# Performance work log

Measured on AMD Instinct MI355X. Metric: run time of the kernel, lower is better.

## Reference

```python
import jax, jax.numpy as jnp
import numpy as np

# static config (matches init_kwargs)
DIM = 192; NUM_HEAD = 6; HEAD_DIM = DIM // NUM_HEAD
WIN = 8; WS = WIN * WIN            # win_seq = 64
B = 2; H = 256; Wd = 256
RH = H // WIN; RW = Wd // WIN; L = RH * RW   # 32x32 = 1024 windows
P = (2 * WIN - 1) ** 2             # 225 relative positions
SCALE = HEAD_DIM ** -0.5


def _relative_index():
    # same math as get_relative_index (torch.meshgrid default = 'ij')
    coords = np.stack(np.meshgrid(np.arange(WIN), np.arange(WIN), indexing='ij'))
    cf = coords.reshape(2, -1)
    rel = (cf[:, :, None] - cf[:, None, :]).transpose(1, 2, 0).copy()
    rel[:, :, 0] += WIN - 1
    rel[:, :, 1] += WIN - 1
    rel[:, :, 0] *= 2 * WIN - 1
    return rel.sum(-1).reshape(-1)  # (WS*WS,), values in [0, P)

POS_INDEX = jnp.asarray(_relative_index())


def _table_nb(rh, rw):
    # reflect-pad(1) + 3x3 unfold of window-id table -> neighbor window ids (L, 9)
    t = np.arange(rh * rw).reshape(rh, rw)
    tp = np.pad(t, 1, mode='reflect')
    nb = np.stack([tp[kh:kh + rh, kw:kw + rw] for kh in range(3) for kw in range(3)], axis=-1)
    return nb.reshape(rh * rw, 9)

TABLE_NB = jnp.asarray(_table_nb(RH, RW))  # (L, 9) int


def _unfold9(x):
    # x: (B, C, rh, rw) -> (B, L, C, 9); reflect pad 1 + 3x3 neighborhoods
    rh, rw = x.shape[2], x.shape[3]
    xp = jnp.pad(x, ((0, 0), (0, 0), (1, 1), (1, 1)), mode='reflect')
    nb = jnp.stack([xp[:, :, kh:kh + rh, kw:kw + rw] for kh in range(3) for kw in range(3)], axis=-1)
    return nb.reshape(x.shape[0], x.shape[1], rh * rw, 9).transpose(0, 2, 1, 3)


def _router(q, k, pos_embedding):
    # router runs on detached q, k (q.detach() in source)
    qd = jax.lax.stop_gradient(q)
    kd = jax.lax.stop_gradient(k)
    qr = qd.reshape(B, DIM, RH, WIN, RW, WIN).mean(axis=(3, 5))
    kr = kd.reshape(B, DIM, RH, WIN, RW, WIN).mean(axis=(3, 5))
    qr_flat = qr.reshape(B, DIM, L).transpose(0, 2, 1)      # (B, L, C)
    kr_fold = _unfold9(kr)                                   # (B, L, C, 9)
    a_r = jnp.einsum('blc,blcn->bln', qr_flat, kr_fold)      # routing scores
    a_r = a_r.at[..., 4].add(-100.0)                          # exclude self window
    # softmax is monotone -> argmax of a_r equals argmax of softmax(a_r)
    idx = jnp.argmax(a_r, axis=-1)                            # (B, L) in [0,9)
    idx_reflect = TABLE_NB[jnp.arange(L)[None, :], idx]       # (B, L) routed window id
    itself = pos_embedding[4]                                 # (nh, P)
    dirb = pos_embedding[idx]                                 # (B, L, nh, P)
    itself_b = itself[:, POS_INDEX].reshape(NUM_HEAD, WS, WS)
    itself_b = jnp.broadcast_to(itself_b, (B, L, NUM_HEAD, WS, WS))
    dir_b = dirb[..., POS_INDEX].reshape(B, L, NUM_HEAD, WS, WS)
    pos_embed = jnp.concatenate([itself_b, dir_b], axis=-1)   # (B, L, nh, WS, 2*WS)
    return idx_reflect, pos_embed


def reference(x, pos_embedding):
    # x: (B, 3*DIM, H, W) fused qkv feature map
    qc = x[:, :DIM]
    kc = x[:, DIM:2 * DIM]
    idx, pos_embed = _router(qc, kc, pos_embedding)
    # winP: window partition into (3, B, L, nh, WS, hd)
    qkv = x.reshape(B, 3, NUM_HEAD, HEAD_DIM, RH, WIN, RW, WIN)
    qkv = qkv.transpose(1, 0, 4, 6, 2, 5, 7, 3).reshape(3, B, L, NUM_HEAD, WS, HEAD_DIM)
    q, k, v = qkv[0], qkv[1], qkv[2]
    gather = jax.vmap(lambda a, i: a[i])     # per-batch window gather along L
    k_d = gather(k, idx)                     # (B, L, nh, WS, hd)
    v_d = gather(v, idx)
    k_g = jnp.concatenate([k, k_d], axis=3)  # (B, L, nh, 2*WS, hd)
    v_g = jnp.concatenate([v, v_d], axis=3)
    attn = jnp.einsum('blhsd,blhtd->blhst', q, k_g) * SCALE + pos_embed
    attn = jax.nn.softmax(attn, axis=-1)
    out = jnp.einsum('blhst,blhtd->blhsd', attn, v_g)  # (B, L, nh, WS, hd)
    # winR: window reverse to (B, DIM, H, W)
    out = out.reshape(B, RH, RW, NUM_HEAD, WIN, WIN, HEAD_DIM)
    out = out.transpose(0, 3, 6, 1, 4, 2, 5).reshape(B, DIM, H, Wd)
    return out


def setup_inputs() -> dict:
    key = jax.random.key(0)
    k1, k2 = jax.random.split(key)
    x = jax.random.normal(k1, (B, 3 * DIM, H, Wd), dtype=jnp.float32)
    pos_embedding = jax.random.normal(k2, (9, NUM_HEAD, P), dtype=jnp.float32) * 0.02
    return {"x": x, "pos_embedding": pos_embedding}
```

## Files before the change

kernel.cpp:

```cpp
#include <hip/hip_runtime.h>
#include <math.h>

namespace {
constexpr int cB   = 2;
constexpr int cDIM = 192;
constexpr int cNH  = 6;
constexpr int cHD  = 32;
constexpr int cWS  = 64;
constexpr int cH   = 256;
constexpr int cW   = 256;
constexpr int cRH  = 32;
constexpr int cL   = 1024;
constexpr int cP   = 225;
constexpr float cSCALE = 0.17677669529663688f;
}

__global__ void pool_kernel(const float* __restrict__ x, float* __restrict__ pool) {
    int blk = blockIdx.x;
    int rh = blk & 31;
    int c  = (blk >> 5) % 384;
    int b  = blk / (384 * 32);
    int tid = threadIdx.x;
    int i  = tid >> 5;
    int rw = tid & 31;
    const float* row = x + (((size_t)(b * 576 + c)) * cH + rh * 8 + i) * cW + rw * 8;
    float4 a0 = *(const float4*)row;
    float4 a1 = *(const float4*)(row + 4);
    float s = a0.x + a0.y + a0.z + a0.w + a1.x + a1.y + a1.z + a1.w;
    __shared__ float red[8][33];
    red[i][rw] = s;
    __syncthreads();
    if (tid < 32) {
        float t = 0.f;
        #pragma unroll
        for (int k = 0; k < 8; ++k) t += red[k][tid];
        pool[((size_t)(b * cL) + rh * 32 + tid) * 384 + c] = t * (1.0f / 64.0f);
    }
}

__global__ void router_kernel(const float* __restrict__ pool, int* __restrict__ idxbuf) {
    int blk = blockIdx.x;
    int l = blk & (cL - 1);
    int b = blk >> 10;
    int rh = l >> 5, rw = l & 31;
    int lane = threadIdx.x;
    int ln[9];
    #pragma unroll
    for (int n = 0; n < 9; ++n) {
        int nh = rh + n / 3 - 1;
        int nw = rw + n % 3 - 1;
        nh = nh < 0 ? 1 : (nh > 31 ? 30 : nh);
        nw = nw < 0 ? 1 : (nw > 31 ? 30 : nw);
        ln[n] = nh * 32 + nw;
    }
    float acc[9] = {0,0,0,0,0,0,0,0,0};
    const float* qb = pool + ((size_t)(b * cL) + l) * 384;
    #pragma unroll
    for (int ci = 0; ci < 3; ++ci) {
        int c = lane + ci * 64;
        float q = qb[c];
        #pragma unroll
        for (int n = 0; n < 9; ++n)
            acc[n] += q * pool[((size_t)(b * cL) + ln[n]) * 384 + 192 + c];
    }
    #pragma unroll
    for (int n = 0; n < 9; ++n)
        #pragma unroll
        for (int off = 32; off > 0; off >>= 1)
            acc[n] += __shfl_down(acc[n], off);
    if (lane == 0) {
        acc[4] -= 100.0f;
        int bi = 0; float bv = acc[0];
        #pragma unroll
        for (int n = 1; n < 9; ++n) if (acc[n] > bv) { bv = acc[n]; bi = n; }
        idxbuf[blk * 2]     = bi;
        idxbuf[blk * 2 + 1] = ln[bi];
    }
}

__global__ __launch_bounds__(256, 2) void attn_kernel(
    const float* __restrict__ x, const float* __restrict__ pe,
    const int* __restrict__ idxbuf, float* __restrict__ out)
{
    __shared__ float smem[12996];
    float* Vs  = smem;
    float* Qs  = smem + 4096;
    float* Ks  = smem + 6144;
    float* Ps  = smem + 4096;
    float* pes = smem + 12544;

    int blk = blockIdx.x;
    int h  = blk >> 11;
    int bl = blk & 2047;
    int b  = bl >> 10;
    int l  = bl & 1023;
    int rh = l >> 5, rw = l & 31;
    int tid = threadIdx.x;

    int dir  = idxbuf[bl * 2];
    int lwin = idxbuf[bl * 2 + 1];
    int rh2 = lwin >> 5, rw2 = lwin & 31;

    const float* pe_self = pe + (4 * cNH + h) * cP;
    const float* pe_dir  = pe + (dir * cNH + h) * cP;
    for (int t = tid; t < 2 * cP; t += 256)
        pes[t] = (t < cP) ? pe_self[t] : pe_dir[t - cP];

    {
        int d = tid & 31;
        int i = tid >> 5;
        int dsw = (d + 4 * i) & 31;
        const size_t CHW = (size_t)cH * cW;
        const float* xb = x + (size_t)b * (3 * cDIM) * CHW;
        size_t off_self = (size_t)(rh  * 8 + i) * cW + rw  * 8;
        size_t off_dir  = (size_t)(rh2 * 8 + i) * cW + rw2 * 8;
        size_t cq = (size_t)(h * cHD + d) * CHW;
        size_t ck = cq + (size_t)cDIM * CHW;
        size_t cv = ck + (size_t)cDIM * CHW;
        const float* srcs[5] = { xb + cq + off_self, xb + ck + off_self, xb + ck + off_dir,
                                 xb + cv + off_self, xb + cv + off_dir };
        float* dsts[5] = { Qs, Ks, Ks + 2048, Vs, Vs + 2048 };
        #pragma unroll
        for (int m = 0; m < 5; ++m) {
            float4 a0 = *(const float4*)(srcs[m]);
            float4 a1 = *(const float4*)(srcs[m] + 4);
            float vv[8] = {a0.x,a0.y,a0.z,a0.w,a1.x,a1.y,a1.z,a1.w};
            float mult = (m == 0) ? cSCALE : 1.0f;
            float* dd = dsts[m] + dsw;
            #pragma unroll
            for (int j = 0; j < 8; ++j)
                dd[(i * 8 + j) * 32] = vv[j] * mult;
        }
    }
    __syncthreads();

    int sg = tid >> 4;
    int tg = tid & 15;
    int s0 = sg * 4;
    int t0 = tg * 8;
    int si = s0 >> 3;
    int sj0 = s0 & 7;

    float sc[4][8];
    {
        const float* peb = pes + ((t0 < 64) ? 0 : cP);
        #pragma unroll
        for (int bb = 0; bb < 8; ++bb) {
            int tw = (t0 + bb) & 63;
            int ti = tw >> 3, tj = tw & 7;
            #pragma unroll
            for (int a = 0; a < 4; ++a)
                sc[a][bb] = peb[(si - ti + 7) * 15 + (sj0 + a - tj + 7)];
        }
    }

    int qc = 4 * (sg >> 1);
    int kc = (4 * tg) & 31;
    #pragma unroll
    for (int d4 = 0; d4 < 32; d4 += 4) {
        float4 qv[4], kv[8];
        #pragma unroll
        for (int a = 0; a < 4; ++a)
            qv[a] = *(const float4*)&Qs[(s0 + a) * 32 + ((d4 + qc) & 31)];
        #pragma unroll
        for (int bb = 0; bb < 8; ++bb)
            kv[bb] = *(const float4*)&Ks[(t0 + bb) * 32 + ((d4 + kc) & 31)];
        #pragma unroll
        for (int a = 0; a < 4; ++a)
            #pragma unroll
            for (int bb = 0; bb < 8; ++bb)
                sc[a][bb] += qv[a].x * kv[bb].x + qv[a].y * kv[bb].y
                           + qv[a].z * kv[bb].z + qv[a].w * kv[bb].w;
    }
    __syncthreads();

    #pragma unroll
    for (int a = 0; a < 4; ++a) {
        float m = sc[a][0];
        #pragma unroll
        for (int bb = 1; bb < 8; ++bb) m = fmaxf(m, sc[a][bb]);
        #pragma unroll
        for (int mask = 1; mask < 16; mask <<= 1) m = fmaxf(m, __shfl_xor(m, mask));
        float ssum = 0.f;
        #pragma unroll
        for (int bb = 0; bb < 8; ++bb) { sc[a][bb] = __expf(sc[a][bb] - m); ssum += sc[a][bb]; }
        #pragma unroll
        for (int mask = 1; mask < 16; mask <<= 1) ssum += __shfl_xor(ssum, mask);
        float r = 1.0f / ssum;
        #pragma unroll
        for (int bb = 0; bb < 8; ++bb) sc[a][bb] *= r;
        *(float4*)&Ps[(s0 + a) * 132 + t0]     = make_float4(sc[a][0], sc[a][1], sc[a][2], sc[a][3]);
        *(float4*)&Ps[(s0 + a) * 132 + t0 + 4] = make_float4(sc[a][4], sc[a][5], sc[a][6], sc[a][7]);
    }
    __syncthreads();

    int d0 = tg * 2;
    float oa0[4] = {0,0,0,0}, oa1[4] = {0,0,0,0};
    for (int t4 = 0; t4 < 128; t4 += 4) {
        int vc = (d0 + 4 * (t4 >> 3)) & 31;
        float4 pv[4];
        #pragma unroll
        for (int a = 0; a < 4; ++a)
            pv[a] = *(const float4*)&Ps[(s0 + a) * 132 + t4];
        float2 vv[4];
        #pragma unroll
        for (int u = 0; u < 4; ++u)
            vv[u] = *(const float2*)&Vs[(t4 + u) * 32 + vc];
        #pragma unroll
        for (int a = 0; a < 4; ++a) {
            oa0[a] += pv[a].x * vv[0].x + pv[a].y * vv[1].x + pv[a].z * vv[2].x + pv[a].w * vv[3].x;
            oa1[a] += pv[a].x * vv[0].y + pv[a].y * vv[1].y + pv[a].z * vv[2].y + pv[a].w * vv[3].y;
        }
    }

    const size_t CHW = (size_t)cH * cW;
    float* ob = out + (size_t)(b * cDIM + h * cHD) * CHW + (size_t)(rh * 8 + si) * cW + rw * 8 + sj0;
    *(float4*)(ob + (size_t)(d0    ) * CHW) = make_float4(oa0[0], oa0[1], oa0[2], oa0[3]);
    *(float4*)(ob + (size_t)(d0 + 1) * CHW) = make_float4(oa1[0], oa1[1], oa1[2], oa1[3]);
}

extern "C" void kernel_launch(void* const* d_in, const int* in_sizes, int n_in,
                              void* d_out, int out_size, void* d_ws, size_t ws_size,
                              hipStream_t stream) {
    const float* x  = (const float*)d_in[0];
    const float* pe = (const float*)d_in[1];
    float* out = (float*)d_out;
    float* pool   = (float*)d_ws;
    int*   idxbuf = (int*)((char*)d_ws + (size_t)cB * cL * 384 * sizeof(float));

    hipLaunchKernelGGL(pool_kernel,   dim3(cB * 384 * cRH), dim3(256), 0, stream, x, pool);
    hipLaunchKernelGGL(router_kernel, dim3(cB * cL),        dim3(64),  0, stream, pool, idxbuf);
    hipLaunchKernelGGL(attn_kernel,   dim3(cNH * cB * cL),  dim3(256), 0, stream, x, pe, idxbuf, out);
}
```

Measured before the change: 656.0 us.

## Use fp16 MFMA for window attention QK and PV products

Replaces the scalar fp32 QK^T and PV loops in the attention kernel with fp16 MFMA 16x16x32 instructions. Q, K and V are staged into shared memory as fp16 (V transposed), and the probability tile is kept per wave. The relative-position bias is loaded directly into the MFMA accumulator, which drops one block barrier. Shared memory shrinks and the launch bound rises to 3 blocks per CU. The cost is reduced precision in the fp16 operands and stores to the output that are no longer vectorized, since each lane now writes scalars.

```diff
diff --git a/kernel.cpp b/kernel.cpp
--- a/kernel.cpp
+++ b/kernel.cpp
@@ -6,7 +6,6 @@
 constexpr int cDIM = 192;
 constexpr int cNH  = 6;
 constexpr int cHD  = 32;
-constexpr int cWS  = 64;
 constexpr int cH   = 256;
 constexpr int cW   = 256;
 constexpr int cRH  = 32;
@@ -14,6 +13,10 @@
 constexpr int cP   = 225;
 constexpr float cSCALE = 0.17677669529663688f;
 }
+
+typedef _Float16 h8 __attribute__((ext_vector_type(8)));
+typedef _Float16 h4 __attribute__((ext_vector_type(4)));
+typedef float    f4 __attribute__((ext_vector_type(4)));
 
 __global__ void pool_kernel(const float* __restrict__ x, float* __restrict__ pool) {
     int blk = blockIdx.x;
@@ -78,16 +81,15 @@
     }
 }
 
-__global__ __launch_bounds__(256, 2) void attn_kernel(
+__global__ __launch_bounds__(256, 3) void attn_kernel(
     const float* __restrict__ x, const float* __restrict__ pe,
     const int* __restrict__ idxbuf, float* __restrict__ out)
 {
-    __shared__ float smem[12996];
-    float* Vs  = smem;
-    float* Qs  = smem + 4096;
-    float* Ks  = smem + 6144;
-    float* Ps  = smem + 4096;
-    float* pes = smem + 12544;
+    __shared__ _Float16 Qh[64 * 40];
+    __shared__ _Float16 Kh[128 * 40];
+    __shared__ _Float16 Vt[32 * 136];
+    __shared__ _Float16 Pst[4][16 * 136];
+    __shared__ float    pes[2 * cP];
 
     int blk = blockIdx.x;
     int h  = blk >> 11;
@@ -109,7 +111,6 @@
     {
         int d = tid & 31;
         int i = tid >> 5;
-        int dsw = (d + 4 * i) & 31;
         const size_t CHW = (size_t)cH * cW;
         const float* xb = x + (size_t)b * (3 * cDIM) * CHW;
         size_t off_self = (size_t)(rh  * 8 + i) * cW + rw  * 8;
@@ -117,106 +118,113 @@
         size_t cq = (size_t)(h * cHD + d) * CHW;
         size_t ck = cq + (size_t)cDIM * CHW;
         size_t cv = ck + (size_t)cDIM * CHW;
-        const float* srcs[5] = { xb + cq + off_self, xb + ck + off_self, xb + ck + off_dir,
-                                 xb + cv + off_self, xb + cv + off_dir };
-        float* dsts[5] = { Qs, Ks, Ks + 2048, Vs, Vs + 2048 };
-        #pragma unroll
-        for (int m = 0; m < 5; ++m) {
-            float4 a0 = *(const float4*)(srcs[m]);
-            float4 a1 = *(const float4*)(srcs[m] + 4);
+
+        {
+            float4 a0 = *(const float4*)(xb + cq + off_self);
+            float4 a1 = *(const float4*)(xb + cq + off_self + 4);
             float vv[8] = {a0.x,a0.y,a0.z,a0.w,a1.x,a1.y,a1.z,a1.w};
-            float mult = (m == 0) ? cSCALE : 1.0f;
-            float* dd = dsts[m] + dsw;
             #pragma unroll
             for (int j = 0; j < 8; ++j)
-                dd[(i * 8 + j) * 32] = vv[j] * mult;
+                Qh[(i * 8 + j) * 40 + d] = (_Float16)(vv[j] * cSCALE);
         }
+        {
+            float4 a0 = *(const float4*)(xb + ck + off_self);
+            float4 a1 = *(const float4*)(xb + ck + off_self + 4);
+            float vv[8] = {a0.x,a0.y,a0.z,a0.w,a1.x,a1.y,a1.z,a1.w};
+            #pragma unroll
+            for (int j = 0; j < 8; ++j)
+                Kh[(i * 8 + j) * 40 + d] = (_Float16)vv[j];
+            float4 b0 = *(const float4*)(xb + ck + off_dir);
+            float4 b1 = *(const float4*)(xb + ck + off_dir + 4);
+            float ww[8] = {b0.x,b0.y,b0.z,b0.w,b1.x,b1.y,b1.z,b1.w};
+            #pragma unroll
+            for (int j = 0; j < 8; ++j)
+                Kh[(64 + i * 8 + j) * 40 + d] = (_Float16)ww[j];
+        }
+        {
+            float4 a0 = *(const float4*)(xb + cv + off_self);
+            float4 a1 = *(const float4*)(xb + cv + off_self + 4);
+            h8 hv = { (_Float16)a0.x,(_Float16)a0.y,(_Float16)a0.z,(_Float16)a0.w,
+                      (_Float16)a1.x,(_Float16)a1.y,(_Float16)a1.z,(_Float16)a1.w };
+            *(h8*)&Vt[d * 136 + i * 8] = hv;
+            float4 b0 = *(const float4*)(xb + cv + off_dir);
+            float4 b1 = *(const float4*)(xb + cv + off_dir + 4);
+            h8 hw = { (_Float16)b0.x,(_Float16)b0.y,(_Float16)b0.z,(_Float16)b0.w,
+                      (_Float16)b1.x,(_Float16)b1.y,(_Float16)b1.z,(_Float16)b1.w };
+            *(h8*)&Vt[d * 136 + 64 + i * 8] = hw;
+        }
     }
     __syncthreads();
 
-    int sg = tid >> 4;
-    int tg = tid & 15;
-    int s0 = sg * 4;
-    int t0 = tg * 8;
-    int si = s0 >> 3;
-    int sj0 = s0 & 7;
-
-    float sc[4][8];
-    {
-        const float* peb = pes + ((t0 < 64) ? 0 : cP);
-        #pragma unroll
-        for (int bb = 0; bb < 8; ++bb) {
-            int tw = (t0 + bb) & 63;
-            int ti = tw >> 3, tj = tw & 7;
-            #pragma unroll
-            for (int a = 0; a < 4; ++a)
-                sc[a][bb] = peb[(si - ti + 7) * 15 + (sj0 + a - tj + 7)];
-        }
-    }
-
-    int qc = 4 * (sg >> 1);
-    int kc = (4 * tg) & 31;
-    #pragma unroll
-    for (int d4 = 0; d4 < 32; d4 += 4) {
-        float4 qv[4], kv[8];
-        #pragma unroll
-        for (int a = 0; a < 4; ++a)
-            qv[a] = *(const float4*)&Qs[(s0 + a) * 32 + ((d4 + qc) & 31)];
-        #pragma unroll
-        for (int bb = 0; bb < 8; ++bb)
-            kv[bb] = *(const float4*)&Ks[(t0 + bb) * 32 + ((d4 + kc) & 31)];
-        #pragma unroll
-        for (int a = 0; a < 4; ++a)
-            #pragma unroll
-            for (int bb = 0; bb < 8; ++bb)
-                sc[a][bb] += qv[a].x * kv[bb].x + qv[a].y * kv[bb].y
-                           + qv[a].z * kv[bb].z + qv[a].w * kv[bb].w;
-    }
-    __syncthreads();
-
-    #pragma unroll
-    for (int a = 0; a < 4; ++a) {
-        float m = sc[a][0];
-        #pragma unroll
-        for (int bb = 1; bb < 8; ++bb) m = fmaxf(m, sc[a][bb]);
-        #pragma unroll
-        for (int mask = 1; mask < 16; mask <<= 1) m = fmaxf(m, __shfl_xor(m, mask));
-        float ssum = 0.f;
-        #pragma unroll
-        for (int bb = 0; bb < 8; ++bb) { sc[a][bb] = __expf(sc[a][bb] - m); ssum += sc[a][bb]; }
-        #pragma unroll
-        for (int mask = 1; mask < 16; mask <<= 1) ssum += __shfl_xor(ssum, mask);
-        float r = 1.0f / ssum;
-        #pragma unroll
-        for (int bb = 0; bb < 8; ++bb) sc[a][bb] *= r;
-        *(float4*)&Ps[(s0 + a) * 132 + t0]     = make_float4(sc[a][0], sc[a][1], sc[a][2], sc[a][3]);
-        *(float4*)&Ps[(s0 + a) * 132 + t0 + 4] = make_float4(sc[a][4], sc[a][5], sc[a][6], sc[a][7]);
-    }
-    __syncthreads();
-
-    int d0 = tg * 2;
-    float oa0[4] = {0,0,0,0}, oa1[4] = {0,0,0,0};
-    for (int t4 = 0; t4 < 128; t4 += 4) {
-        int vc = (d0 + 4 * (t4 >> 3)) & 31;
-        float4 pv[4];
-        #pragma unroll
-        for (int a = 0; a < 4; ++a)
-            pv[a] = *(const float4*)&Ps[(s0 + a) * 132 + t4];
-        float2 vv[4];
-        #pragma unroll
-        for (int u = 0; u < 4; ++u)
-            vv[u] = *(const float2*)&Vs[(t4 + u) * 32 + vc];
-        #pragma unroll
-        for (int a = 0; a < 4; ++a) {
-            oa0[a] += pv[a].x * vv[0].x + pv[a].y * vv[1].x + pv[a].z * vv[2].x + pv[a].w * vv[3].x;
-            oa1[a] += pv[a].x * vv[0].y + pv[a].y * vv[1].y + pv[a].z * vv[2].y + pv[a].w * vv[3].y;
-        }
+    int lane = tid & 63;
+    int w    = tid >> 6;
+    int g    = lane >> 4;
+    int sl   = lane & 15;
+    int s_global = w * 16 + sl;
+
+    int base0 = ((s_global >> 3) + 7) * 15 + (s_global & 7) + 7;
+    int offs[4];
+    #pragma unroll
+    for (int q = 0; q < 4; ++q) {
+        int gq = 4 * g + q;
+        offs[q] = (gq >> 3) * 15 + (gq & 7);
+    }
+
+    h8 qf = *(const h8*)&Qh[s_global * 40 + g * 8];
+    f4 ST[8];
+    #pragma unroll
+    for (int T = 0; T < 8; ++T) {
+        int base = ((T < 4) ? 0 : cP) + base0 - (T & 3) * 30;
+        f4 c;
+        #pragma unroll
+        for (int q = 0; q < 4; ++q) c[q] = pes[base - offs[q]];
+        h8 kf = *(const h8*)&Kh[(T * 16 + sl) * 40 + g * 8];
+        ST[T] = __builtin_amdgcn_mfma_f32_16x16x32_f16(kf, qf, c, 0, 0, 0);
+    }
+
+    float mx = -1e30f;
+    #pragma unroll
+    for (int T = 0; T < 8; ++T)
+        #pragma unroll
+        for (int q = 0; q < 4; ++q) mx = fmaxf(mx, ST[T][q]);
+    mx = fmaxf(mx, __shfl_xor(mx, 16));
+    mx = fmaxf(mx, __shfl_xor(mx, 32));
+    float sum = 0.f;
+    #pragma unroll
+    for (int T = 0; T < 8; ++T)
+        #pragma unroll
+        for (int q = 0; q < 4; ++q) { float e = __expf(ST[T][q] - mx); ST[T][q] = e; sum += e; }
+    sum += __shfl_xor(sum, 16);
+    sum += __shfl_xor(sum, 32);
+    float r = 1.0f / sum;
+
+    _Float16* prow = &Pst[w][sl * 136];
+    #pragma unroll
+    for (int T = 0; T < 8; ++T) {
+        h4 p = { (_Float16)(ST[T][0] * r), (_Float16)(ST[T][1] * r),
+                 (_Float16)(ST[T][2] * r), (_Float16)(ST[T][3] * r) };
+        *(h4*)&prow[T * 16 + g * 4] = p;
+    }
+
+    f4 O0 = {0.f,0.f,0.f,0.f}, O1 = {0.f,0.f,0.f,0.f};
+    #pragma unroll
+    for (int kb = 0; kb < 4; ++kb) {
+        h8 pf = *(const h8*)&Pst[w][sl * 136 + kb * 32 + g * 8];
+        h8 v0 = *(const h8*)&Vt[ sl       * 136 + kb * 32 + g * 8];
+        h8 v1 = *(const h8*)&Vt[(16 + sl) * 136 + kb * 32 + g * 8];
+        O0 = __builtin_amdgcn_mfma_f32_16x16x32_f16(v0, pf, O0, 0, 0, 0);
+        O1 = __builtin_amdgcn_mfma_f32_16x16x32_f16(v1, pf, O1, 0, 0, 0);
     }
 
     const size_t CHW = (size_t)cH * cW;
-    float* ob = out + (size_t)(b * cDIM + h * cHD) * CHW + (size_t)(rh * 8 + si) * cW + rw * 8 + sj0;
-    *(float4*)(ob + (size_t)(d0    ) * CHW) = make_float4(oa0[0], oa0[1], oa0[2], oa0[3]);
-    *(float4*)(ob + (size_t)(d0 + 1) * CHW) = make_float4(oa1[0], oa1[1], oa1[2], oa1[3]);
+    int pr = rh * 8 + (s_global >> 3);
+    int pc = rw * 8 + (s_global & 7);
+    float* ob = out + ((size_t)(b * cDIM + h * cHD)) * CHW + (size_t)pr * cW + pc;
+    #pragma unroll
+    for (int q = 0; q < 4; ++q) {
+        ob[(size_t)(4 * g + q) * CHW]      = O0[q];
+        ob[(size_t)(16 + 4 * g + q) * CHW] = O1[q];
+    }
 }
 
 extern "C" void kernel_launch(void* const* d_in, const int* in_sizes, int n_in,
```

Result: faster. 610.8 us (-6.9%).
